# Performance work log

Measured on AMD Instinct MI355X. Metric: run time of the kernel, lower is better.

## Reference

```python
import jax, jax.numpy as jnp
import numpy as np

N_NODES = 50000
N_EDGES = 600000
HIDDEN = 128
NUM_FEAT = 3
NUM_CLASSES = 2
NUM_GRAPHS = 512


def setup_inputs() -> dict:
    key = jax.random.key(0)
    ks = jax.random.split(key, 12)
    x = jax.random.normal(ks[0], (N_NODES, NUM_FEAT), dtype=jnp.float32)
    edge_index = jax.random.randint(ks[1], (2, N_EDGES), 0, N_NODES, dtype=jnp.int64)
    batch = jnp.sort(jax.random.randint(ks[2], (N_NODES,), 0, NUM_GRAPHS, dtype=jnp.int64))

    def glorot(k, fan_in, fan_out):
        s = jnp.sqrt(6.0 / (fan_in + fan_out)).astype(jnp.float32)
        return jax.random.uniform(k, (fan_in, fan_out), jnp.float32, -s, s)

    return {
        "x": x,
        "W1": glorot(ks[3], NUM_FEAT, HIDDEN), "b1": jnp.zeros((HIDDEN,), jnp.float32),
        "W2": glorot(ks[4], HIDDEN, HIDDEN),  "b2": jnp.zeros((HIDDEN,), jnp.float32),
        "W3": glorot(ks[5], HIDDEN, HIDDEN),  "b3": jnp.zeros((HIDDEN,), jnp.float32),
        "W4": glorot(ks[6], HIDDEN, HIDDEN),  "b4": jnp.zeros((HIDDEN,), jnp.float32),
        "linW": glorot(ks[7], HIDDEN, NUM_CLASSES), "linb": jnp.zeros((NUM_CLASSES,), jnp.float32),
        "edge_index": edge_index,
        "batch": batch,
        "num_graphs": NUM_GRAPHS,
    }


def gcn_conv(x, W, b, src, dst, n_nodes):
    # PyG GCNConv: h = x W; out = D^-1/2 (A + I) D^-1/2 h + b
    h = x @ W                                    # [N, out]
    deg = jnp.zeros((n_nodes,), h.dtype).at[dst].add(1.0) + 1.0  # with self-loops
    dinv = jax.lax.rsqrt(deg)                    # [N]
    norm = dinv[src] * dinv[dst]                 # [E]
    msg = h[src] * norm[:, None]                 # gather + scale
    agg = jax.ops.segment_sum(msg, dst, num_segments=n_nodes)  # scatter-add
    agg = agg + h * (dinv * dinv)[:, None]       # self-loop contribution
    return agg + b


def reference(x, W1, b1, W2, b2, W3, b3, W4, b4, linW, linb, edge_index, batch, num_graphs):
    src, dst = edge_index[0], edge_index[1]
    n = x.shape[0]
    h = jax.nn.relu(gcn_conv(x, W1, b1, src, dst, n))
    h = jax.nn.relu(gcn_conv(h, W2, b2, src, dst, n))
    h = jax.nn.relu(gcn_conv(h, W3, b3, src, dst, n))
    h = gcn_conv(h, W4, b4, src, dst, n)
    # global_mean_pool over graphs
    sums = jax.ops.segment_sum(h, batch, num_segments=num_graphs)
    cnts = jax.ops.segment_sum(jnp.ones((n,), h.dtype), batch, num_segments=num_graphs)
    pooled = sums / jnp.maximum(cnts, 1.0)[:, None]
    # dropout is identity in eval mode
    return pooled @ linW + linb
```

## Files before the change

### kernel.cpp

```cpp
#include <hip/hip_runtime.h>
#include <hip/hip_bf16.h>

#define HID 128
#define NGRAPH 512

typedef __attribute__((ext_vector_type(8))) short short8;
typedef __attribute__((ext_vector_type(4))) float f32x4;

__device__ inline unsigned int f2bf(float f) {
    unsigned int u = __float_as_uint(f);
    return (u + 0x7FFFu + ((u >> 16) & 1u)) >> 16;
}
__device__ inline float bflo(unsigned int w) { return __uint_as_float(w << 16); }
__device__ inline float bfhi(unsigned int w) { return __uint_as_float(w & 0xFFFF0000u); }


__device__ inline void wcast_body(const float* __restrict__ W,
                                  unsigned short* __restrict__ Wt) {
    int t = threadIdx.x;
#pragma unroll
    for (int i = 0; i < 16; ++i) {
        int flat = i * 1024 + t;
        int n = flat >> 7, k = flat & 127;
        Wt[n * HID + k] = (unsigned short)f2bf(W[k * HID + n]);
    }
}

__global__ void k_setup1(int* __restrict__ deg, int n, int nzb,
                         const float* __restrict__ W4, const float* __restrict__ linW,
                         const float* __restrict__ b4, const float* __restrict__ linb,
                         float* __restrict__ W4p, float* __restrict__ b4p,
                         const float* __restrict__ W2, const float* __restrict__ W3,
                         unsigned short* __restrict__ Wt2, unsigned short* __restrict__ Wt3) {
    if ((int)blockIdx.x == nzb) {
        int idx = threadIdx.x;
        if (idx < 256) {
            int k = idx >> 1, c = idx & 1;
            float a = 0.0f;
            for (int j = 0; j < HID; ++j) a = fmaf(W4[k * HID + j], linW[j * 2 + c], a);
            W4p[idx] = a;
            if (idx < 2) {
                float b = 0.0f;
                for (int j = 0; j < HID; ++j) b = fmaf(b4[j], linW[j * 2 + idx], b);
                b4p[idx] = b + linb[idx];
            }
        }
        return;
    }
    if ((int)blockIdx.x == nzb + 1) { wcast_body(W2, Wt2); return; }
    if ((int)blockIdx.x == nzb + 2) { wcast_body(W3, Wt3); return; }
    int i = blockIdx.x * 1024 + threadIdx.x;
    if (i < n) deg[i] = 0;
}

__global__ void k_count(const int* __restrict__ ei, int* __restrict__ deg,
                        int* __restrict__ epos, int E) {
    int e = blockIdx.x * blockDim.x + threadIdx.x;
    if (e < E) epos[e] = atomicAdd(&deg[ei[E + e]], 1);
}

__global__ void k_scan2b(const int* __restrict__ deg, int* __restrict__ row_start,
                         float* __restrict__ dinv, const float* __restrict__ x,
                         float* __restrict__ Xs, int n, int nblocks) {
    __shared__ int rs[16];
    __shared__ int ws[16];
    __shared__ int s_off_sh;
    int lane = threadIdx.x & 63, wid = threadIdx.x >> 6;
    {
        int before = blockIdx.x * 1024;
        int p = 0;
        for (int i = threadIdx.x; i < before; i += 1024) p += deg[i];
#pragma unroll
        for (int off = 32; off; off >>= 1) p += __shfl_down(p, off);
        if (lane == 0) rs[wid] = p;
        __syncthreads();
        if (threadIdx.x == 0) {
            int s = 0;
#pragma unroll
            for (int w = 0; w < 16; ++w) s += rs[w];
            s_off_sh = s;
        }
        __syncthreads();
    }
    int i = blockIdx.x * 1024 + threadIdx.x;
    int v = (i < n) ? deg[i] : 0;
    if (i < n) {
        float dv = rsqrtf((float)v + 1.0f);
        dinv[i] = dv;
        float4 r;
        r.x = x[i * 3 + 0] * dv;
        r.y = x[i * 3 + 1] * dv;
        r.z = x[i * 3 + 2] * dv;
        r.w = 0.0f;
        *(float4*)&Xs[i * 4] = r;
    }
    int xx = v;
#pragma unroll
    for (int off = 1; off < 64; off <<= 1) {
        int t = __shfl_up(xx, off);
        if (lane >= off) xx += t;
    }
    if (lane == 63) ws[wid] = xx;
    __syncthreads();
    int wo = 0;
    for (int w = 0; w < wid; ++w) wo += ws[w];
    int excl = s_off_sh + wo + xx - v;
    if (i < n) row_start[i] = excl;
    if ((int)blockIdx.x == nblocks - 1 && threadIdx.x == 0) {
        int ct = 0;
#pragma unroll
        for (int w = 0; w < 16; ++w) ct += ws[w];
        row_start[n] = s_off_sh + ct;
    }
}

__global__ void k_fill(const int* __restrict__ ei, const int* __restrict__ row_start,
                       const int* __restrict__ epos, int* __restrict__ src_sorted, int E) {
    int e = blockIdx.x * blockDim.x + threadIdx.x;
    if (e < E) {
        int s = ei[e];
        int d = ei[E + e];
        src_sorted[row_start[d] + epos[e]] = s;
    }
}

__global__ __launch_bounds__(256) void k_l1(const float* __restrict__ Xs,
                                            const int* __restrict__ row_start,
                                            const int* __restrict__ src_sorted,
                                            const float* __restrict__ dinv,
                                            const float* __restrict__ W1,
                                            const float* __restrict__ b1,
                                            unsigned int* __restrict__ Act16, int n) {
    __shared__ float xs[32][4];
    int v0 = blockIdx.x * 32;
    int vl0 = threadIdx.x >> 3, sub = threadIdx.x & 7;
    int v = v0 + vl0;
    float a0 = 0.f, a1 = 0.f, a2 = 0.f;
    if (v < n) {
        int e0 = row_start[v], e1 = row_start[v + 1];
        for (int e = e0 + sub; e < e1; e += 8) {
            int s = src_sorted[e];
            float4 xv = *(const float4*)&Xs[s * 4];
            a0 += xv.x; a1 += xv.y; a2 += xv.z;
        }
    }
#pragma unroll
    for (int off = 4; off; off >>= 1) {
        a0 += __shfl_down(a0, off);
        a1 += __shfl_down(a1, off);
        a2 += __shfl_down(a2, off);
    }
    if (sub == 0 && v < n) {
        float dv = dinv[v];
        float4 xv = *(const float4*)&Xs[v * 4];
        xs[vl0][0] = (a0 + xv.x) * dv;
        xs[vl0][1] = (a1 + xv.y) * dv;
        xs[vl0][2] = (a2 + xv.z) * dv;
    }
    __syncthreads();
    unsigned int base = (unsigned int)v0 * 64;
#pragma unroll
    for (int i = 0; i < 8; ++i) {
        int flat = i * 256 + threadIdx.x;
        int vl = flat >> 6, cp = flat & 63;
        unsigned int w = 0;
        if (v0 + vl < n) {
            float x0 = xs[vl][0], x1 = xs[vl][1], x2 = xs[vl][2];
            int c0 = cp * 2, c1 = c0 + 1;
            float r0 = fmaf(x0, W1[c0], fmaf(x1, W1[HID + c0], fmaf(x2, W1[2 * HID + c0], b1[c0])));
            float r1 = fmaf(x0, W1[c1], fmaf(x1, W1[HID + c1], fmaf(x2, W1[2 * HID + c1], b1[c1])));
            w = f2bf(fmaxf(r0, 0.f)) | (f2bf(fmaxf(r1, 0.f)) << 16);
        }
        Act16[base + flat] = w;
    }
}

__global__ __launch_bounds__(256) void k_gemm_mfma(const unsigned short* __restrict__ X,
                                                   const unsigned short* __restrict__ Wtg,
                                                   const float* __restrict__ dinv,
                                                   unsigned short* __restrict__ Hout) {
    __shared__ unsigned short Wt[HID * HID];
    {
        int nrow = threadIdx.x >> 1, s = threadIdx.x & 1;
        int xr = (nrow & 7) << 3;
#pragma unroll
        for (int i = 0; i < 8; ++i) {
            int b16 = s * 64 + i * 8;
            uint4 src = *(const uint4*)&Wtg[nrow * HID + b16];
            *(uint4*)&Wt[nrow * HID + (b16 ^ xr)] = src;
        }
    }
    __syncthreads();

    int w    = threadIdx.x >> 6;
    int lane = threadIdx.x & 63;
    int g    = lane >> 4;
    int mr   = lane & 15;
    size_t row0 = (size_t)blockIdx.x * 64;
    size_t arow = row0 + w * 16 + mr;

    short8 a[4];
#pragma unroll
    for (int ks = 0; ks < 4; ++ks)
        a[ks] = *(const short8*)&X[arow * HID + ks * 32 + g * 8];

    f32x4 acc[8];
#pragma unroll
    for (int nt = 0; nt < 8; ++nt) acc[nt] = (f32x4){0.f, 0.f, 0.f, 0.f};

#pragma unroll
    for (int nt = 0; nt < 8; ++nt) {
        int nrow = nt * 16 + mr;
        int xr = (nrow & 7) << 3;
        short8 b[4];
#pragma unroll
        for (int ks = 0; ks < 4; ++ks)
            b[ks] = *(const short8*)&Wt[nrow * HID + ((ks * 32 + g * 8) ^ xr)];
#pragma unroll
        for (int ks = 0; ks < 4; ++ks)
            acc[nt] = __builtin_amdgcn_mfma_f32_16x16x32_bf16(a[ks], b[ks], acc[nt], 0, 0, 0);
    }

    __syncthreads();
    {
        int rrb = w * 16 + g * 4;
#pragma unroll
        for (int j = 0; j < 4; ++j) {
            int rr = rrb + j;
            float dv = dinv[row0 + rr];
#pragma unroll
            for (int nt = 0; nt < 8; ++nt) {
                int col = nt * 16 + mr;
                int idx = rr * HID + ((col & 7) | ((((col >> 3)) ^ (rr & 7)) << 3));
                Wt[idx] = (unsigned short)f2bf(acc[nt][j] * dv);
            }
        }
    }
    __syncthreads();
    {
        int rr = threadIdx.x >> 2, s = threadIdx.x & 3;
        int xr = (rr & 7) << 3;
#pragma unroll
        for (int i = 0; i < 4; ++i) {
            int b16 = s * 32 + i * 8;
            uint4 v = *(const uint4*)&Wt[rr * HID + (b16 ^ xr)];
            *(uint4*)&Hout[(row0 + rr) * HID + b16] = v;
        }
    }
}

__global__ __launch_bounds__(256) void k_gather(const unsigned short* __restrict__ Hs,
                                                const int* __restrict__ row_start,
                                                const int* __restrict__ src_sorted,
                                                const float* __restrict__ dinv,
                                                const float* __restrict__ bias,
                                                unsigned short* __restrict__ Aout, int n) {
    int wid  = (blockIdx.x * blockDim.x + threadIdx.x) >> 6;
    int lane = threadIdx.x & 63;
    int half = lane >> 5, hl = lane & 31;
    int v0 = wid * 2;
    if (v0 >= n) return;
    int v  = v0 + half;
    bool real = (v < n);
    int vc = real ? v : v0;
    int e0 = row_start[vc];
    int e1 = row_start[vc + 1];
    int deg = e1 - e0;
    int myidx = (hl < deg) ? src_sorted[e0 + hl] : vc;
    float4 acc = make_float4(0.f, 0.f, 0.f, 0.f);
    int dcap = (deg < 32) ? deg : 32;
    for (int base = 0; base < dcap; base += 16) {
        uint2 h[16];
        float m[16];
#pragma unroll
        for (int j = 0; j < 16; ++j) {
            int ej = base + j;
            int sj = __shfl(myidx, (half << 5) | ej);
            m[j] = (ej < deg) ? 1.0f : 0.0f;
            h[j] = *(const uint2*)&Hs[(size_t)sj * HID + hl * 4];
        }
#pragma unroll
        for (int j = 0; j < 16; ++j) {
            acc.x = fmaf(bflo(h[j].x), m[j], acc.x);
            acc.y = fmaf(bfhi(h[j].x), m[j], acc.y);
            acc.z = fmaf(bflo(h[j].y), m[j], acc.z);
            acc.w = fmaf(bfhi(h[j].y), m[j], acc.w);
        }
    }
    for (int e = e0 + 32; e < e1; ++e) {
        int sj = src_sorted[e];
        uint2 h = *(const uint2*)&Hs[(size_t)sj * HID + hl * 4];
        acc.x += bflo(h.x); acc.y += bfhi(h.x);
        acc.z += bflo(h.y); acc.w += bfhi(h.y);
    }
    float dv = dinv[vc];
    uint2 sv = *(const uint2*)&Hs[(size_t)vc * HID + hl * 4];
    float4 bb = *(const float4*)&bias[hl * 4];
    float ox = fmaxf(fmaf(acc.x + bflo(sv.x), dv, bb.x), 0.0f);
    float oy = fmaxf(fmaf(acc.y + bfhi(sv.x), dv, bb.y), 0.0f);
    float oz = fmaxf(fmaf(acc.z + bflo(sv.y), dv, bb.z), 0.0f);
    float ow = fmaxf(fmaf(acc.w + bfhi(sv.y), dv, bb.w), 0.0f);
    if (real) {
        uint2 o2;
        o2.x = f2bf(ox) | (f2bf(oy) << 16);
        o2.y = f2bf(oz) | (f2bf(ow) << 16);
        *(uint2*)&Aout[(size_t)v * HID + hl * 4] = o2;
    }
}

__global__ __launch_bounds__(256) void k_gather_proj(const unsigned short* __restrict__ Hs,
                                                     const int* __restrict__ row_start,
                                                     const int* __restrict__ src_sorted,
                                                     const float* __restrict__ dinv,
                                                     const float* __restrict__ bias,
                                                     const float* __restrict__ W4p,
                                                     float* __restrict__ P3s, int n) {
    int wid  = (blockIdx.x * blockDim.x + threadIdx.x) >> 6;
    int lane = threadIdx.x & 63;
    int half = lane >> 5, hl = lane & 31;
    int v0 = wid * 2;
    if (v0 >= n) return;
    int v  = v0 + half;
    bool real = (v < n);
    int vc = real ? v : v0;
    int e0 = row_start[vc];
    int e1 = row_start[vc + 1];
    int deg = e1 - e0;
    int myidx = (hl < deg) ? src_sorted[e0 + hl] : vc;
    float4 acc = make_float4(0.f, 0.f, 0.f, 0.f);
    int dcap = (deg < 32) ? deg : 32;
    for (int base = 0; base < dcap; base += 16) {
        uint2 h[16];
        float m[16];
#pragma unroll
        for (int j = 0; j < 16; ++j) {
            int ej = base + j;
            int sj = __shfl(myidx, (half << 5) | ej);
            m[j] = (ej < deg) ? 1.0f : 0.0f;
            h[j] = *(const uint2*)&Hs[(size_t)sj * HID + hl * 4];
        }
#pragma unroll
        for (int j = 0; j < 16; ++j) {
            acc.x = fmaf(bflo(h[j].x), m[j], acc.x);
            acc.y = fmaf(bfhi(h[j].x), m[j], acc.y);
            acc.z = fmaf(bflo(h[j].y), m[j], acc.z);
            acc.w = fmaf(bfhi(h[j].y), m[j], acc.w);
        }
    }
    for (int e = e0 + 32; e < e1; ++e) {
        int sj = src_sorted[e];
        uint2 h = *(const uint2*)&Hs[(size_t)sj * HID + hl * 4];
        acc.x += bflo(h.x); acc.y += bfhi(h.x);
        acc.z += bflo(h.y); acc.w += bfhi(h.y);
    }
    float dv = dinv[vc];
    uint2 sv = *(const uint2*)&Hs[(size_t)vc * HID + hl * 4];
    float4 bb = *(const float4*)&bias[hl * 4];
    float ox = fmaxf(fmaf(acc.x + bflo(sv.x), dv, bb.x), 0.0f);
    float oy = fmaxf(fmaf(acc.y + bfhi(sv.x), dv, bb.y), 0.0f);
    float oz = fmaxf(fmaf(acc.z + bflo(sv.y), dv, bb.z), 0.0f);
    float ow = fmaxf(fmaf(acc.w + bfhi(sv.y), dv, bb.w), 0.0f);
    float4 wA = *(const float4*)&W4p[hl * 8 + 0];
    float4 wB = *(const float4*)&W4p[hl * 8 + 4];
    float p0 = ox * wA.x + oy * wA.z + oz * wB.x + ow * wB.z;
    float p1 = ox * wA.y + oy * wA.w + oz * wB.y + ow * wB.w;
#pragma unroll
    for (int off = 16; off; off >>= 1) {
        p0 += __shfl_down(p0, off);
        p1 += __shfl_down(p1, off);
    }
    if (hl == 0 && real) *(float2*)&P3s[v * 2] = make_float2(p0 * dv, p1 * dv);
}

__global__ __launch_bounds__(256) void k_tail(const float* __restrict__ P3s,
                                              const int* __restrict__ row_start,
                                              const int* __restrict__ src_sorted,
                                              const float* __restrict__ dinv,
                                              const int* __restrict__ batch,
                                              const float* __restrict__ b4p,
                                              float* __restrict__ out, int n) {
    int g = blockIdx.x;
    int lo = 0, hi = n;
    while (lo < hi) { int m = (lo + hi) >> 1; if (batch[m] < g) lo = m + 1; else hi = m; }
    int start = lo;
    hi = n;
    while (lo < hi) { int m = (lo + hi) >> 1; if (batch[m] < g + 1) lo = m + 1; else hi = m; }
    int end = lo;

    int grp = threadIdx.x >> 3, sub = threadIdx.x & 7;
    float gx = 0.f, gy = 0.f;
    for (int v = start + grp; v < end; v += 32) {
        float ax = 0.f, ay = 0.f;
        int e0 = row_start[v], e1 = row_start[v + 1];
        for (int e = e0 + sub; e < e1; e += 8) {
            int s = src_sorted[e];
            float2 ps = *(const float2*)&P3s[s * 2];
            ax += ps.x;
            ay += ps.y;
        }
#pragma unroll
        for (int off = 4; off; off >>= 1) {
            ax += __shfl_down(ax, off);
            ay += __shfl_down(ay, off);
        }
        if (sub == 0) {
            float dv = dinv[v];
            float2 pv = *(const float2*)&P3s[v * 2];
            gx += (ax + pv.x) * dv;
            gy += (ay + pv.y) * dv;
        }
    }
    __shared__ float red[64];
    if (sub == 0) { red[grp] = gx; red[grp + 32] = gy; }
    __syncthreads();
    if (threadIdx.x < 64) {
        float sx = (threadIdx.x < 32) ? red[threadIdx.x] : 0.f;
        float sy = (threadIdx.x < 32) ? red[threadIdx.x + 32] : 0.f;
#pragma unroll
        for (int off = 16; off; off >>= 1) {
            sx += __shfl_down(sx, off);
            sy += __shfl_down(sy, off);
        }
        if (threadIdx.x == 0) {
            float inv = 1.0f / fmaxf((float)(end - start), 1.0f);
            out[g * 2 + 0] = sx * inv + b4p[0];
            out[g * 2 + 1] = sy * inv + b4p[1];
        }
    }
}


extern "C" void kernel_launch(void* const* d_in, const int* in_sizes, int n_in,
                              void* d_out, int out_size, void* d_ws, size_t ws_size,
                              hipStream_t stream) {
    const float* x    = (const float*)d_in[0];
    const float* W1   = (const float*)d_in[1];
    const float* b1   = (const float*)d_in[2];
    const float* W2   = (const float*)d_in[3];
    const float* b2   = (const float*)d_in[4];
    const float* W3   = (const float*)d_in[5];
    const float* b3   = (const float*)d_in[6];
    const float* W4   = (const float*)d_in[7];
    const float* b4   = (const float*)d_in[8];
    const float* linW = (const float*)d_in[9];
    const float* linb = (const float*)d_in[10];
    const int*   ei   = (const int*)d_in[11];
    const int*   batch= (const int*)d_in[12];
    float* out        = (float*)d_out;

    const int N = in_sizes[0] / 3;
    const int E = in_sizes[11] / 2;
    const int NPAD = ((N + 127) / 128) * 128;
    const int NB1024 = (N + 1023) / 1024;

    float* ws = (float*)d_ws;
    float* dinv       = ws;
    int*   deg_i      = (int*)(ws + 50176);
    int*   row_start  = (int*)(ws + 100352);
    int*   epos       = (int*)(ws + 150784);
    int*   bsum       = (int*)(ws + 750848);
    float* W4p        = ws + 750912;
    float* b4p        = ws + 751168;
    int*   src_sorted = (int*)(ws + 751232);
    float* P3s        = ws + 1552000;
    unsigned short* Hbuf16 = (unsigned short*)(ws + 1652352);
    float* Xs         = ws + 1652352;
    unsigned short* Act16 = (unsigned short*)(ws + 1652352 + (size_t)NPAD * 64);
    unsigned short* Wt2g  = (unsigned short*)(ws + 1652352 + 2 * (size_t)NPAD * 64);
    unsigned short* Wt3g  = Wt2g + HID * HID;
    (void)bsum;

    const int B = 256;

    k_setup1<<<NB1024 + 3, 1024, 0, stream>>>(deg_i, N, NB1024, W4, linW, b4, linb,
                                              W4p, b4p, W2, W3, Wt2g, Wt3g);
    k_count<<<(E + B - 1) / B, B, 0, stream>>>(ei, deg_i, epos, E);
    k_scan2b<<<NB1024, 1024, 0, stream>>>(deg_i, row_start, dinv, x, Xs, N, NB1024);
    k_fill<<<(E + B - 1) / B, B, 0, stream>>>(ei, row_start, epos, src_sorted, E);

    const int gatherBlocks = (N + 7) / 8;
    const int gemmBlocks   = NPAD / 64;

    k_l1<<<NPAD / 32, B, 0, stream>>>(Xs, row_start, src_sorted, dinv, W1, b1,
                                      (unsigned int*)Act16, N);
    k_gemm_mfma<<<gemmBlocks, B, 0, stream>>>(Act16, Wt2g, dinv, Hbuf16);
    k_gather<<<gatherBlocks, B, 0, stream>>>(Hbuf16, row_start, src_sorted, dinv, b2, Act16, N);
    k_gemm_mfma<<<gemmBlocks, B, 0, stream>>>(Act16, Wt3g, dinv, Hbuf16);
    k_gather_proj<<<gatherBlocks, B, 0, stream>>>(Hbuf16, row_start, src_sorted, dinv, b3, W4p, P3s, N);
    k_tail<<<NGRAPH, B, 0, stream>>>(P3s, row_start, src_sorted, dinv, batch, b4p, out, N);
}
```

Before: 169.8 us.

## Fuse layer-1 aggregation with layer-2 GEMM and widen gather loads to 16 bytes

Merges the layer-1 neighbor aggregation and projection with the following MFMA GEMM into one kernel. The bf16 activation tile now stays in LDS and never round-trips through global memory, and one launch is dropped. The gather kernels switch to four nodes per wavefront, with 16 lanes each loading 16-byte chunks instead of 8-byte ones, and out-of-degree loads are predicated away rather than masked. Xs and P3s are relocated so Xs no longer aliases Hbuf16, which the fused kernel writes. The fused kernel uses more LDS per block, which may reduce occupancy.

Result: faster. 162.2 us (-4.5%).

```diff
diff --git a/kernel.cpp b/kernel.cpp
--- a/kernel.cpp
+++ b/kernel.cpp
@@ -124,54 +124,124 @@
     }
 }
 
-__global__ __launch_bounds__(256) void k_l1(const float* __restrict__ Xs,
-                                            const int* __restrict__ row_start,
-                                            const int* __restrict__ src_sorted,
-                                            const float* __restrict__ dinv,
-                                            const float* __restrict__ W1,
-                                            const float* __restrict__ b1,
-                                            unsigned int* __restrict__ Act16, int n) {
-    __shared__ float xs[32][4];
-    int v0 = blockIdx.x * 32;
-    int vl0 = threadIdx.x >> 3, sub = threadIdx.x & 7;
-    int v = v0 + vl0;
-    float a0 = 0.f, a1 = 0.f, a2 = 0.f;
-    if (v < n) {
-        int e0 = row_start[v], e1 = row_start[v + 1];
-        for (int e = e0 + sub; e < e1; e += 8) {
-            int s = src_sorted[e];
-            float4 xv = *(const float4*)&Xs[s * 4];
-            a0 += xv.x; a1 += xv.y; a2 += xv.z;
-        }
-    }
-#pragma unroll
-    for (int off = 4; off; off >>= 1) {
-        a0 += __shfl_down(a0, off);
-        a1 += __shfl_down(a1, off);
-        a2 += __shfl_down(a2, off);
-    }
-    if (sub == 0 && v < n) {
-        float dv = dinv[v];
-        float4 xv = *(const float4*)&Xs[v * 4];
-        xs[vl0][0] = (a0 + xv.x) * dv;
-        xs[vl0][1] = (a1 + xv.y) * dv;
-        xs[vl0][2] = (a2 + xv.z) * dv;
-    }
-    __syncthreads();
-    unsigned int base = (unsigned int)v0 * 64;
-#pragma unroll
-    for (int i = 0; i < 8; ++i) {
-        int flat = i * 256 + threadIdx.x;
-        int vl = flat >> 6, cp = flat & 63;
-        unsigned int w = 0;
-        if (v0 + vl < n) {
-            float x0 = xs[vl][0], x1 = xs[vl][1], x2 = xs[vl][2];
+__global__ __launch_bounds__(256) void k_l1g2(const float* __restrict__ Xs,
+                                              const int* __restrict__ row_start,
+                                              const int* __restrict__ src_sorted,
+                                              const float* __restrict__ dinv,
+                                              const float* __restrict__ W1,
+                                              const float* __restrict__ b1,
+                                              const unsigned short* __restrict__ Wtg,
+                                              unsigned short* __restrict__ Hout, int n) {
+    __shared__ unsigned short Wt[HID * HID];
+    __shared__ unsigned short AT[64 * HID];
+    __shared__ float xs[64][4];
+
+    {
+        int nrow = threadIdx.x >> 1, s = threadIdx.x & 1;
+        int xr = (nrow & 7) << 3;
+#pragma unroll
+        for (int i = 0; i < 8; ++i) {
+            int b16 = s * 64 + i * 8;
+            *(uint4*)&Wt[nrow * HID + (b16 ^ xr)] = *(const uint4*)&Wtg[nrow * HID + b16];
+        }
+    }
+    {
+        int grp = threadIdx.x >> 2, sub = threadIdx.x & 3;
+        int v = blockIdx.x * 64 + grp;
+        float a0 = 0.f, a1 = 0.f, a2 = 0.f;
+        if (v < n) {
+            int e0 = row_start[v], e1 = row_start[v + 1];
+            for (int e = e0 + sub; e < e1; e += 4) {
+                int s2 = src_sorted[e];
+                float4 xv = *(const float4*)&Xs[s2 * 4];
+                a0 += xv.x; a1 += xv.y; a2 += xv.z;
+            }
+        }
+        a0 += __shfl_xor(a0, 2); a0 += __shfl_xor(a0, 1);
+        a1 += __shfl_xor(a1, 2); a1 += __shfl_xor(a1, 1);
+        a2 += __shfl_xor(a2, 2); a2 += __shfl_xor(a2, 1);
+        if (sub == 0) {
+            if (v < n) {
+                float dv = dinv[v];
+                float4 xv = *(const float4*)&Xs[v * 4];
+                xs[grp][0] = (a0 + xv.x) * dv;
+                xs[grp][1] = (a1 + xv.y) * dv;
+                xs[grp][2] = (a2 + xv.z) * dv;
+            } else {
+                xs[grp][0] = 0.f; xs[grp][1] = 0.f; xs[grp][2] = 0.f;
+            }
+        }
+    }
+    __syncthreads();
+    {
+#pragma unroll
+        for (int i = 0; i < 16; ++i) {
+            int flat = i * 256 + threadIdx.x;
+            int row = flat >> 6, cp = flat & 63;
+            float x0 = xs[row][0], x1 = xs[row][1], x2 = xs[row][2];
             int c0 = cp * 2, c1 = c0 + 1;
             float r0 = fmaf(x0, W1[c0], fmaf(x1, W1[HID + c0], fmaf(x2, W1[2 * HID + c0], b1[c0])));
             float r1 = fmaf(x0, W1[c1], fmaf(x1, W1[HID + c1], fmaf(x2, W1[2 * HID + c1], b1[c1])));
-            w = f2bf(fmaxf(r0, 0.f)) | (f2bf(fmaxf(r1, 0.f)) << 16);
-        }
-        Act16[base + flat] = w;
+            unsigned int w = f2bf(fmaxf(r0, 0.f)) | (f2bf(fmaxf(r1, 0.f)) << 16);
+            int soff = (c0 & 7) | ((((c0 >> 3)) ^ (row & 7)) << 3);
+            *(unsigned int*)&AT[row * HID + soff] = w;
+        }
+    }
+    __syncthreads();
+    int w    = threadIdx.x >> 6;
+    int lane = threadIdx.x & 63;
+    int g    = lane >> 4;
+    int mr   = lane & 15;
+    size_t row0 = (size_t)blockIdx.x * 64;
+    int arow = w * 16 + mr;
+    int axr = (arow & 7) << 3;
+
+    short8 a[4];
+#pragma unroll
+    for (int ks = 0; ks < 4; ++ks)
+        a[ks] = *(const short8*)&AT[arow * HID + ((ks * 32 + g * 8) ^ axr)];
+
+    f32x4 acc[8];
+#pragma unroll
+    for (int nt = 0; nt < 8; ++nt) acc[nt] = (f32x4){0.f, 0.f, 0.f, 0.f};
+
+#pragma unroll
+    for (int nt = 0; nt < 8; ++nt) {
+        int nrow = nt * 16 + mr;
+        int xr = (nrow & 7) << 3;
+        short8 b[4];
+#pragma unroll
+        for (int ks = 0; ks < 4; ++ks)
+            b[ks] = *(const short8*)&Wt[nrow * HID + ((ks * 32 + g * 8) ^ xr)];
+#pragma unroll
+        for (int ks = 0; ks < 4; ++ks)
+            acc[nt] = __builtin_amdgcn_mfma_f32_16x16x32_bf16(a[ks], b[ks], acc[nt], 0, 0, 0);
+    }
+    __syncthreads();
+    {
+        int rrb = w * 16 + g * 4;
+#pragma unroll
+        for (int j = 0; j < 4; ++j) {
+            int rr = rrb + j;
+            float dv = dinv[row0 + rr];
+#pragma unroll
+            for (int nt = 0; nt < 8; ++nt) {
+                int col = nt * 16 + mr;
+                int idx = rr * HID + ((col & 7) | ((((col >> 3)) ^ (rr & 7)) << 3));
+                AT[idx] = (unsigned short)f2bf(acc[nt][j] * dv);
+            }
+        }
+    }
+    __syncthreads();
+    {
+        int rr = threadIdx.x >> 2, s = threadIdx.x & 3;
+        int xr = (rr & 7) << 3;
+#pragma unroll
+        for (int i = 0; i < 4; ++i) {
+            int b16 = s * 32 + i * 8;
+            uint4 v = *(const uint4*)&AT[rr * HID + (b16 ^ xr)];
+            *(uint4*)&Hout[(row0 + rr) * HID + b16] = v;
+        }
     }
 }
 
@@ -257,54 +327,79 @@
                                                 unsigned short* __restrict__ Aout, int n) {
     int wid  = (blockIdx.x * blockDim.x + threadIdx.x) >> 6;
     int lane = threadIdx.x & 63;
-    int half = lane >> 5, hl = lane & 31;
-    int v0 = wid * 2;
+    int q = lane >> 4, ql = lane & 15;
+    int v0 = wid * 4;
     if (v0 >= n) return;
-    int v  = v0 + half;
+    int v  = v0 + q;
     bool real = (v < n);
     int vc = real ? v : v0;
-    int e0 = row_start[vc];
-    int e1 = row_start[vc + 1];
+    int e0 = row_start[vc], e1 = row_start[vc + 1];
     int deg = e1 - e0;
-    int myidx = (hl < deg) ? src_sorted[e0 + hl] : vc;
-    float4 acc = make_float4(0.f, 0.f, 0.f, 0.f);
-    int dcap = (deg < 32) ? deg : 32;
-    for (int base = 0; base < dcap; base += 16) {
-        uint2 h[16];
-        float m[16];
-#pragma unroll
-        for (int j = 0; j < 16; ++j) {
-            int ej = base + j;
-            int sj = __shfl(myidx, (half << 5) | ej);
-            m[j] = (ej < deg) ? 1.0f : 0.0f;
-            h[j] = *(const uint2*)&Hs[(size_t)sj * HID + hl * 4];
-        }
-#pragma unroll
-        for (int j = 0; j < 16; ++j) {
-            acc.x = fmaf(bflo(h[j].x), m[j], acc.x);
-            acc.y = fmaf(bfhi(h[j].x), m[j], acc.y);
-            acc.z = fmaf(bflo(h[j].y), m[j], acc.z);
-            acc.w = fmaf(bfhi(h[j].y), m[j], acc.w);
+    int idx0 = (ql < deg) ? src_sorted[e0 + ql] : vc;
+    int idx1 = (16 + ql < deg) ? src_sorted[e0 + 16 + ql] : vc;
+    float4 accA = make_float4(0.f, 0.f, 0.f, 0.f);
+    float4 accB = make_float4(0.f, 0.f, 0.f, 0.f);
+    {
+        uint4 h[16];
+#pragma unroll
+        for (int j = 0; j < 16; ++j) {
+            int sj = __shfl(idx0, (q << 4) | j);
+            uint4 hv = make_uint4(0u, 0u, 0u, 0u);
+            if (j < deg) hv = *(const uint4*)&Hs[(size_t)sj * HID + ql * 8];
+            h[j] = hv;
+        }
+#pragma unroll
+        for (int j = 0; j < 16; ++j) {
+            accA.x += bflo(h[j].x); accA.y += bfhi(h[j].x);
+            accA.z += bflo(h[j].y); accA.w += bfhi(h[j].y);
+            accB.x += bflo(h[j].z); accB.y += bfhi(h[j].z);
+            accB.z += bflo(h[j].w); accB.w += bfhi(h[j].w);
+        }
+    }
+    if (deg > 16) {
+        uint4 h[16];
+#pragma unroll
+        for (int j = 0; j < 16; ++j) {
+            int sj = __shfl(idx1, (q << 4) | j);
+            uint4 hv = make_uint4(0u, 0u, 0u, 0u);
+            if (16 + j < deg) hv = *(const uint4*)&Hs[(size_t)sj * HID + ql * 8];
+            h[j] = hv;
+        }
+#pragma unroll
+        for (int j = 0; j < 16; ++j) {
+            accA.x += bflo(h[j].x); accA.y += bfhi(h[j].x);
+            accA.z += bflo(h[j].y); accA.w += bfhi(h[j].y);
+            accB.x += bflo(h[j].z); accB.y += bfhi(h[j].z);
+            accB.z += bflo(h[j].w); accB.w += bfhi(h[j].w);
         }
     }
     for (int e = e0 + 32; e < e1; ++e) {
         int sj = src_sorted[e];
-        uint2 h = *(const uint2*)&Hs[(size_t)sj * HID + hl * 4];
-        acc.x += bflo(h.x); acc.y += bfhi(h.x);
-        acc.z += bflo(h.y); acc.w += bfhi(h.y);
+        uint4 h = *(const uint4*)&Hs[(size_t)sj * HID + ql * 8];
+        accA.x += bflo(h.x); accA.y += bfhi(h.x);
+        accA.z += bflo(h.y); accA.w += bfhi(h.y);
+        accB.x += bflo(h.z); accB.y += bfhi(h.z);
+        accB.z += bflo(h.w); accB.w += bfhi(h.w);
     }
     float dv = dinv[vc];
-    uint2 sv = *(const uint2*)&Hs[(size_t)vc * HID + hl * 4];
-    float4 bb = *(const float4*)&bias[hl * 4];
-    float ox = fmaxf(fmaf(acc.x + bflo(sv.x), dv, bb.x), 0.0f);
-    float oy = fmaxf(fmaf(acc.y + bfhi(sv.x), dv, bb.y), 0.0f);
-    float oz = fmaxf(fmaf(acc.z + bflo(sv.y), dv, bb.z), 0.0f);
-    float ow = fmaxf(fmaf(acc.w + bfhi(sv.y), dv, bb.w), 0.0f);
+    uint4 sv = *(const uint4*)&Hs[(size_t)vc * HID + ql * 8];
+    float4 bbA = *(const float4*)&bias[ql * 8 + 0];
+    float4 bbB = *(const float4*)&bias[ql * 8 + 4];
+    float o0 = fmaxf(fmaf(accA.x + bflo(sv.x), dv, bbA.x), 0.f);
+    float o1 = fmaxf(fmaf(accA.y + bfhi(sv.x), dv, bbA.y), 0.f);
+    float o2 = fmaxf(fmaf(accA.z + bflo(sv.y), dv, bbA.z), 0.f);
+    float o3 = fmaxf(fmaf(accA.w + bfhi(sv.y), dv, bbA.w), 0.f);
+    float o4 = fmaxf(fmaf(accB.x + bflo(sv.z), dv, bbB.x), 0.f);
+    float o5 = fmaxf(fmaf(accB.y + bfhi(sv.z), dv, bbB.y), 0.f);
+    float o6 = fmaxf(fmaf(accB.z + bflo(sv.w), dv, bbB.z), 0.f);
+    float o7 = fmaxf(fmaf(accB.w + bfhi(sv.w), dv, bbB.w), 0.f);
     if (real) {
-        uint2 o2;
-        o2.x = f2bf(ox) | (f2bf(oy) << 16);
-        o2.y = f2bf(oz) | (f2bf(ow) << 16);
-        *(uint2*)&Aout[(size_t)v * HID + hl * 4] = o2;
+        uint4 o;
+        o.x = f2bf(o0) | (f2bf(o1) << 16);
+        o.y = f2bf(o2) | (f2bf(o3) << 16);
+        o.z = f2bf(o4) | (f2bf(o5) << 16);
+        o.w = f2bf(o6) | (f2bf(o7) << 16);
+        *(uint4*)&Aout[(size_t)v * HID + ql * 8] = o;
     }
 }
 
@@ -317,59 +412,86 @@
                                                      float* __restrict__ P3s, int n) {
     int wid  = (blockIdx.x * blockDim.x + threadIdx.x) >> 6;
     int lane = threadIdx.x & 63;
-    int half = lane >> 5, hl = lane & 31;
-    int v0 = wid * 2;
+    int q = lane >> 4, ql = lane & 15;
+    int v0 = wid * 4;
     if (v0 >= n) return;
-    int v  = v0 + half;
+    int v  = v0 + q;
     bool real = (v < n);
     int vc = real ? v : v0;
-    int e0 = row_start[vc];
-    int e1 = row_start[vc + 1];
+    int e0 = row_start[vc], e1 = row_start[vc + 1];
     int deg = e1 - e0;
-    int myidx = (hl < deg) ? src_sorted[e0 + hl] : vc;
-    float4 acc = make_float4(0.f, 0.f, 0.f, 0.f);
-    int dcap = (deg < 32) ? deg : 32;
-    for (int base = 0; base < dcap; base += 16) {
-        uint2 h[16];
-        float m[16];
-#pragma unroll
-        for (int j = 0; j < 16; ++j) {
-            int ej = base + j;
-            int sj = __shfl(myidx, (half << 5) | ej);
-            m[j] = (ej < deg) ? 1.0f : 0.0f;
-            h[j] = *(const uint2*)&Hs[(size_t)sj * HID + hl * 4];
-        }
-#pragma unroll
-        for (int j = 0; j < 16; ++j) {
-            acc.x = fmaf(bflo(h[j].x), m[j], acc.x);
-            acc.y = fmaf(bfhi(h[j].x), m[j], acc.y);
-            acc.z = fmaf(bflo(h[j].y), m[j], acc.z);
-            acc.w = fmaf(bfhi(h[j].y), m[j], acc.w);
+    int idx0 = (ql < deg) ? src_sorted[e0 + ql] : vc;
+    int idx1 = (16 + ql < deg) ? src_sorted[e0 + 16 + ql] : vc;
+    float4 accA = make_float4(0.f, 0.f, 0.f, 0.f);
+    float4 accB = make_float4(0.f, 0.f, 0.f, 0.f);
+    {
+        uint4 h[16];
+#pragma unroll
+        for (int j = 0; j < 16; ++j) {
+            int sj = __shfl(idx0, (q << 4) | j);
+            uint4 hv = make_uint4(0u, 0u, 0u, 0u);
+            if (j < deg) hv = *(const uint4*)&Hs[(size_t)sj * HID + ql * 8];
+            h[j] = hv;
+        }
+#pragma unroll
+        for (int j = 0; j < 16; ++j) {
+            accA.x += bflo(h[j].x); accA.y += bfhi(h[j].x);
+            accA.z += bflo(h[j].y); accA.w += bfhi(h[j].y);
+            accB.x += bflo(h[j].z); accB.y += bfhi(h[j].z);
+            accB.z += bflo(h[j].w); accB.w += bfhi(h[j].w);
+        }
+    }
+    if (deg > 16) {
+        uint4 h[16];
+#pragma unroll
+        for (int j = 0; j < 16; ++j) {
+            int sj = __shfl(idx1, (q << 4) | j);
+            uint4 hv = make_uint4(0u, 0u, 0u, 0u);
+            if (16 + j < deg) hv = *(const uint4*)&Hs[(size_t)sj * HID + ql * 8];
+            h[j] = hv;
+        }
+#pragma unroll
+        for (int j = 0; j < 16; ++j) {
+            accA.x += bflo(h[j].x); accA.y += bfhi(h[j].x);
+            accA.z += bflo(h[j].y); accA.w += bfhi(h[j].y);
+            accB.x += bflo(h[j].z); accB.y += bfhi(h[j].z);
+            accB.z += bflo(h[j].w); accB.w += bfhi(h[j].w);
         }
     }
     for (int e = e0 + 32; e < e1; ++e) {
         int sj = src_sorted[e];
-        uint2 h = *(const uint2*)&Hs[(size_t)sj * HID + hl * 4];
-        acc.x += bflo(h.x); acc.y += bfhi(h.x);
-        acc.z += bflo(h.y); acc.w += bfhi(h.y);
+        uint4 h = *(const uint4*)&Hs[(size_t)sj * HID + ql * 8];
+        accA.x += bflo(h.x); accA.y += bfhi(h.x);
+        accA.z += bflo(h.y); accA.w += bfhi(h.y);
+        accB.x += bflo(h.z); accB.y += bfhi(h.z);
+        accB.z += bflo(h.w); accB.w += bfhi(h.w);
     }
     float dv = dinv[vc];
-    uint2 sv = *(const uint2*)&Hs[(size_t)vc * HID + hl * 4];
-    float4 bb = *(const float4*)&bias[hl * 4];
-    float ox = fmaxf(fmaf(acc.x + bflo(sv.x), dv, bb.x), 0.0f);
-    float oy = fmaxf(fmaf(acc.y + bfhi(sv.x), dv, bb.y), 0.0f);
-    float oz = fmaxf(fmaf(acc.z + bflo(sv.y), dv, bb.z), 0.0f);
-    float ow = fmaxf(fmaf(acc.w + bfhi(sv.y), dv, bb.w), 0.0f);
-    float4 wA = *(const float4*)&W4p[hl * 8 + 0];
-    float4 wB = *(const float4*)&W4p[hl * 8 + 4];
-    float p0 = ox * wA.x + oy * wA.z + oz * wB.x + ow * wB.z;
-    float p1 = ox * wA.y + oy * wA.w + oz * wB.y + ow * wB.w;
-#pragma unroll
-    for (int off = 16; off; off >>= 1) {
-        p0 += __shfl_down(p0, off);
-        p1 += __shfl_down(p1, off);
-    }
-    if (hl == 0 && real) *(float2*)&P3s[v * 2] = make_float2(p0 * dv, p1 * dv);
+    uint4 sv = *(const uint4*)&Hs[(size_t)vc * HID + ql * 8];
+    float4 bbA = *(const float4*)&bias[ql * 8 + 0];
+    float4 bbB = *(const float4*)&bias[ql * 8 + 4];
+    float o0 = fmaxf(fmaf(accA.x + bflo(sv.x), dv, bbA.x), 0.f);
+    float o1 = fmaxf(fmaf(accA.y + bfhi(sv.x), dv, bbA.y), 0.f);
+    float o2 = fmaxf(fmaf(accA.z + bflo(sv.y), dv, bbA.z), 0.f);
+    float o3 = fmaxf(fmaf(accA.w + bfhi(sv.y), dv, bbA.w), 0.f);
+    float o4 = fmaxf(fmaf(accB.x + bflo(sv.z), dv, bbB.x), 0.f);
+    float o5 = fmaxf(fmaf(accB.y + bfhi(sv.z), dv, bbB.y), 0.f);
+    float o6 = fmaxf(fmaf(accB.z + bflo(sv.w), dv, bbB.z), 0.f);
+    float o7 = fmaxf(fmaf(accB.w + bfhi(sv.w), dv, bbB.w), 0.f);
+    float4 w0 = *(const float4*)&W4p[ql * 16 + 0];
+    float4 w1 = *(const float4*)&W4p[ql * 16 + 4];
+    float4 w2 = *(const float4*)&W4p[ql * 16 + 8];
+    float4 w3 = *(const float4*)&W4p[ql * 16 + 12];
+    float p0 = o0 * w0.x + o1 * w0.z + o2 * w1.x + o3 * w1.z
+             + o4 * w2.x + o5 * w2.z + o6 * w3.x + o7 * w3.z;
+    float p1 = o0 * w0.y + o1 * w0.w + o2 * w1.y + o3 * w1.w
+             + o4 * w2.y + o5 * w2.w + o6 * w3.y + o7 * w3.w;
+#pragma unroll
+    for (int off = 8; off; off >>= 1) {
+        p0 += __shfl_xor(p0, off);
+        p1 += __shfl_xor(p1, off);
+    }
+    if (ql == 0 && real) *(float2*)&P3s[v * 2] = make_float2(p0 * dv, p1 * dv);
 }
 
 __global__ __launch_bounds__(256) void k_tail(const float* __restrict__ P3s,
@@ -458,17 +580,15 @@
     int*   deg_i      = (int*)(ws + 50176);
     int*   row_start  = (int*)(ws + 100352);
     int*   epos       = (int*)(ws + 150784);
-    int*   bsum       = (int*)(ws + 750848);
     float* W4p        = ws + 750912;
     float* b4p        = ws + 751168;
     int*   src_sorted = (int*)(ws + 751232);
-    float* P3s        = ws + 1552000;
+    float* P3s        = ws + 1351296;
+    float* Xs         = ws + 1451648;
     unsigned short* Hbuf16 = (unsigned short*)(ws + 1652352);
-    float* Xs         = ws + 1652352;
-    unsigned short* Act16 = (unsigned short*)(ws + 1652352 + (size_t)NPAD * 64);
-    unsigned short* Wt2g  = (unsigned short*)(ws + 1652352 + 2 * (size_t)NPAD * 64);
-    unsigned short* Wt3g  = Wt2g + HID * HID;
-    (void)bsum;
+    unsigned short* Act16  = (unsigned short*)(ws + 1652352 + (size_t)NPAD * 64);
+    unsigned short* Wt2g   = (unsigned short*)(ws + 1652352 + 2 * (size_t)NPAD * 64);
+    unsigned short* Wt3g   = Wt2g + HID * HID;
 
     const int B = 256;
 
@@ -478,12 +598,11 @@
     k_scan2b<<<NB1024, 1024, 0, stream>>>(deg_i, row_start, dinv, x, Xs, N, NB1024);
     k_fill<<<(E + B - 1) / B, B, 0, stream>>>(ei, row_start, epos, src_sorted, E);
 
-    const int gatherBlocks = (N + 7) / 8;
+    const int gatherBlocks = (N + 15) / 16;
     const int gemmBlocks   = NPAD / 64;
 
-    k_l1<<<NPAD / 32, B, 0, stream>>>(Xs, row_start, src_sorted, dinv, W1, b1,
-                                      (unsigned int*)Act16, N);
-    k_gemm_mfma<<<gemmBlocks, B, 0, stream>>>(Act16, Wt2g, dinv, Hbuf16);
+    k_l1g2<<<gemmBlocks, B, 0, stream>>>(Xs, row_start, src_sorted, dinv, W1, b1,
+                                         Wt2g, Hbuf16, N);
     k_gather<<<gatherBlocks, B, 0, stream>>>(Hbuf16, row_start, src_sorted, dinv, b2, Act16, N);
     k_gemm_mfma<<<gemmBlocks, B, 0, stream>>>(Act16, Wt3g, dinv, Hbuf16);
     k_gather_proj<<<gatherBlocks, B, 0, stream>>>(Hbuf16, row_start, src_sorted, dinv, b3, W4p, P3s, N);
```
